# Optimization experiments

Measured on AMD Instinct MI355X. Metric: run time of the kernel, lower is better.

The kernel has to match this reference:

```python
import jax, jax.numpy as jnp
import numpy as np

# YOLOv4 stride-8 head config (yolov4.cfg)
ALL_ANCHORS = [[12,16],[19,36],[40,28],[36,75],[76,55],[72,146],[142,110],[192,243],[459,401]]
ANCHOR_MASK = [0, 1, 2]
N_CLASSES = 80
SCALE_XY = 1.2  # scale_x_y for this head
N_BBOX_ATTRS = 5  # tx, ty, tw, th, obj


def setup_inputs() -> dict:
    key = jax.random.key(0)
    attrs = N_CLASSES + N_BBOX_ATTRS  # 85
    n_anchors = len(ANCHOR_MASK)      # 3
    # raw conv output: [batch, n_anchors*attrs, grid, grid]
    x = jax.random.normal(key, (16, n_anchors * attrs, 76, 76), dtype=jnp.float32)
    return {"x": x, "input_dim": 608}


def reference(x, input_dim):
    B = x.shape[0]
    G = x.shape[2]                      # grid_dim (INPUT_H_DIM)
    stride = input_dim // G             # grid_stride
    A = len(ANCHOR_MASK)
    attrs = N_CLASSES + N_BBOX_ATTRS

    # anchors scaled to grid units: [A, 2]
    anc = jnp.asarray([ALL_ANCHORS[i] for i in ANCHOR_MASK], dtype=jnp.float32) / stride

    # [B, A, attrs, H, W] -> [B, H, W, A, attrs]
    x = x.reshape(B, A, attrs, G, G).transpose(0, 3, 4, 1, 2)

    # yolo_transform: sigmoid+scale tx/ty, exp*anchor tw/th, sigmoid obj+cls
    txy = jax.nn.sigmoid(x[..., 0:2]) * SCALE_XY - (SCALE_XY - 1.0) / 2.0
    twh = jnp.exp(x[..., 2:4]) * anc            # broadcast over [B,H,W,A,2]
    objcls = jax.nn.sigmoid(x[..., 4:])

    # add_grid_offsets: torch.meshgrid(grid, grid) is 'ij' -> y_offset[i,j]=i, x_offset[i,j]=j
    gy, gx = jnp.meshgrid(jnp.arange(G), jnp.arange(G), indexing="ij")
    off = jnp.stack([gx, gy], axis=-1).astype(jnp.float32)[:, :, None, :]  # [H,W,1,2]
    txy = txy + off

    # scale bbox attrs (tx..th) to input-image pixels
    boxes = jnp.concatenate([txy, twh], axis=-1) * jnp.float32(stride)

    out = jnp.concatenate([boxes, objcls], axis=-1)  # [B,H,W,A,attrs]
    return out.reshape(B, G * G * A, attrs)
```

## Files before the change

### kernel.cpp

```cpp
#include <hip/hip_runtime.h>

#define GRIDD  76
#define NROWS  255
#define GG     (GRIDD * GRIDD)
#define WR     16
#define WQ     (WR * 19)
#define WDW    (WR * GRIDD)

typedef __attribute__((address_space(3))) unsigned lds_u32;
typedef __attribute__((address_space(1))) unsigned glb_u32;

__device__ __forceinline__ void gll16(const float* g, float* l) {
    __builtin_amdgcn_global_load_lds((const glb_u32*)g, (lds_u32*)l, 16, 0, 0);
}

__global__ __launch_bounds__(512, 8) void yolo_head_kernel(
    const float* __restrict__ x, const int* __restrict__ dimp,
    float* __restrict__ out)
{
    __shared__ float buf[8 * WDW];
    const unsigned lb    = (blockIdx.x & 7u) * 304u + (blockIdx.x >> 3);
    const unsigned b     = lb / 152u;
    const unsigned hr    = lb - b * 152u;
    const unsigned h     = hr >> 1;
    const unsigned rbase = (hr & 1u) * 127u;
    const unsigned t     = threadIdx.x;
    const unsigned W     = t >> 6;
    const unsigned lane  = t & 63u;
    const float stride   = (float)(*dimp / GRIDD);
    const float mB       = -0.1f * stride;

    float* wbuf = buf + W * WDW;
    const unsigned wr0 = rbase + W * WR;
    const float* __restrict__ src = x + (size_t)(b * NROWS + wr0) * GG + h * GRIDD;
    #pragma unroll
    for (unsigned k = 0; k < 5u; ++k) {
        unsigned i = k * 64u + lane;
        if (i < WQ) {
            unsigned row = i / 19u;
            unsigned qc  = i - row * 19u;
            gll16(src + (size_t)row * GG + (qc << 2), wbuf + k * 256u);
        }
    }
    asm volatile("s_waitcnt vmcnt(0)" ::: "memory");

    const unsigned r    = lane & 15u;
    const unsigned rem  = wr0 + r;
    const unsigned a    = (rem >= 170u) ? 2u : ((rem >= 85u) ? 1u : 0u);
    const unsigned attr = rem - a * 85u;
    const bool  wh  = (attr == 2u) | (attr == 3u);
    const bool  isx = (attr == 0u);
    float anc = 0.f;
    if (attr == 2u) anc = (a == 0u) ? 12.f : ((a == 1u) ? 19.f : 40.f);
    if (attr == 3u) anc = (a == 0u) ? 16.f : ((a == 1u) ? 36.f : 28.f);
    const float sgn = wh ? 1.f : -1.f;
    const float A   = (attr < 2u) ? 1.2f * stride : 1.f;
    const float B0  = (attr == 1u) ? ((float)h * stride + mB) : 0.f;

    const float* lr = wbuf + r * GRIDD;
    float* __restrict__ dst = out + (size_t)(b * GRIDD + h) * (GRIDD * NROWS) + rem;

    #pragma unroll
    for (unsigned j = 0; j < 5u; ++j) {
        const unsigned qj = (lane >> 4) + (j << 2);
        if (qj < 19u) {
            const float4 vv = *reinterpret_cast<const float4*>(lr + (qj << 2));
            #pragma unroll
            for (unsigned i = 0; i < 4u; ++i) {
                const float v = (i == 0) ? vv.x : (i == 1) ? vv.y : (i == 2) ? vv.z : vv.w;
                const unsigned u = (qj << 2) + i;
                const float e   = __expf(sgn * v);
                const float sig = __builtin_amdgcn_rcpf(1.0f + e);
                const float Bi  = isx ? fmaf((float)u, stride, mB) : B0;
                const float o   = wh ? e * anc : fmaf(sig, A, Bi);
                dst[(size_t)u * NROWS] = o;
            }
        }
    }
}

extern "C" void kernel_launch(void* const* d_in, const int* in_sizes, int n_in,
                              void* d_out, int out_size, void* d_ws, size_t ws_size,
                              hipStream_t stream) {
    const float* x  = (const float*)d_in[0];
    const int* dimp = (const int*)d_in[1];
    float* out      = (float*)d_out;
    const int B = in_sizes[0] / (NROWS * GG);
    yolo_head_kernel<<<B * GRIDD * 2, 512, 0, stream>>>(x, dimp, out);
}
```

Measured before the change: 34.06 us.

## Stage block rows in two halves and overlap the second load with compute

After: 37.56 us. 10.3% more time.

```diff
diff --git a/kernel.cpp b/kernel.cpp
--- a/kernel.cpp
+++ b/kernel.cpp
@@ -3,9 +3,9 @@
 #define GRIDD  76
 #define NROWS  255
 #define GG     (GRIDD * GRIDD)
-#define WR     16
-#define WQ     (WR * 19)
-#define WDW    (WR * GRIDD)
+#define HROWS  64
+#define UPITCH 76
+#define UDW    (2 * HROWS * UPITCH)
 
 typedef __attribute__((address_space(3))) unsigned lds_u32;
 typedef __attribute__((address_space(1))) unsigned glb_u32;
@@ -14,38 +14,35 @@
     __builtin_amdgcn_global_load_lds((const glb_u32*)g, (lds_u32*)l, 16, 0, 0);
 }
 
-__global__ __launch_bounds__(512, 8) void yolo_head_kernel(
-    const float* __restrict__ x, const int* __restrict__ dimp,
-    float* __restrict__ out)
+__device__ __forceinline__ void stage_half(const float* __restrict__ src,
+                                           float* dstbase,
+                                           unsigned wid, unsigned lane)
 {
-    __shared__ float buf[8 * WDW];
-    const unsigned lb    = (blockIdx.x & 7u) * 304u + (blockIdx.x >> 3);
-    const unsigned b     = lb / 152u;
-    const unsigned hr    = lb - b * 152u;
-    const unsigned h     = hr >> 1;
-    const unsigned rbase = (hr & 1u) * 127u;
-    const unsigned t     = threadIdx.x;
-    const unsigned W     = t >> 6;
-    const unsigned lane  = t & 63u;
-    const float stride   = (float)(*dimp / GRIDD);
-    const float mB       = -0.1f * stride;
-
-    float* wbuf = buf + W * WDW;
-    const unsigned wr0 = rbase + W * WR;
-    const float* __restrict__ src = x + (size_t)(b * NROWS + wr0) * GG + h * GRIDD;
     #pragma unroll
-    for (unsigned k = 0; k < 5u; ++k) {
-        unsigned i = k * 64u + lane;
-        if (i < WQ) {
+    for (unsigned k = 0; k < 2u; ++k) {
+        unsigned i   = k * 512u + (wid << 6) + lane;
+        unsigned row = i / 19u;
+        unsigned qc  = i - row * 19u;
+        gll16(src + (size_t)row * GG + (qc << 2),
+              dstbase + (size_t)(k * 512u + (wid << 6)) * 4u);
+    }
+    {
+        unsigned i = 1024u + wid * 24u + lane;
+        if (lane < 24u) {
             unsigned row = i / 19u;
             unsigned qc  = i - row * 19u;
-            gll16(src + (size_t)row * GG + (qc << 2), wbuf + k * 256u);
+            gll16(src + (size_t)row * GG + (qc << 2),
+                  dstbase + (size_t)(1024u + wid * 24u) * 4u);
         }
     }
-    asm volatile("s_waitcnt vmcnt(0)" ::: "memory");
+}
 
-    const unsigned r    = lane & 15u;
-    const unsigned rem  = wr0 + r;
+__device__ __forceinline__ void compute_half(const float* __restrict__ bc,
+                                             float* __restrict__ outbh,
+                                             unsigned remBase, unsigned lane,
+                                             unsigned wid, float stride, float fh)
+{
+    const unsigned rem  = remBase + lane;
     const unsigned a    = (rem >= 170u) ? 2u : ((rem >= 85u) ? 1u : 0u);
     const unsigned attr = rem - a * 85u;
     const bool  wh  = (attr == 2u) | (attr == 3u);
@@ -53,30 +50,60 @@
     float anc = 0.f;
     if (attr == 2u) anc = (a == 0u) ? 12.f : ((a == 1u) ? 19.f : 40.f);
     if (attr == 3u) anc = (a == 0u) ? 16.f : ((a == 1u) ? 36.f : 28.f);
-    const float sgn = wh ? 1.f : -1.f;
-    const float A   = (attr < 2u) ? 1.2f * stride : 1.f;
-    const float B0  = (attr == 1u) ? ((float)h * stride + mB) : 0.f;
-
-    const float* lr = wbuf + r * GRIDD;
-    float* __restrict__ dst = out + (size_t)(b * GRIDD + h) * (GRIDD * NROWS) + rem;
+    const float mB    = -0.1f * stride;
+    const float slog  = wh ? 1.44269504f : -1.44269504f;
+    const float A2    = wh ? anc : ((attr < 2u) ? 1.2f * stride : 1.f);
+    const float wsel  = isx ? stride : 0.f;
+    const float basef = (attr == 1u) ? fmaf(fh, stride, mB) : (isx ? mB : 0.f);
+    float* __restrict__ dst = outbh + rem;
 
     #pragma unroll
-    for (unsigned j = 0; j < 5u; ++j) {
-        const unsigned qj = (lane >> 4) + (j << 2);
-        if (qj < 19u) {
-            const float4 vv = *reinterpret_cast<const float4*>(lr + (qj << 2));
+    for (unsigned j = 0; j < 3u; ++j) {
+        const unsigned tt = wid + (j << 3);
+        if (tt < 19u) {
+            const float4 vv = *reinterpret_cast<const float4*>(
+                bc + (size_t)lane * UPITCH + (tt << 2));
             #pragma unroll
             for (unsigned i = 0; i < 4u; ++i) {
-                const float v = (i == 0) ? vv.x : (i == 1) ? vv.y : (i == 2) ? vv.z : vv.w;
-                const unsigned u = (qj << 2) + i;
-                const float e   = __expf(sgn * v);
-                const float sig = __builtin_amdgcn_rcpf(1.0f + e);
-                const float Bi  = isx ? fmaf((float)u, stride, mB) : B0;
-                const float o   = wh ? e * anc : fmaf(sig, A, Bi);
-                dst[(size_t)u * NROWS] = o;
+                const float v  = (i == 0) ? vv.x : (i == 1) ? vv.y : (i == 2) ? vv.z : vv.w;
+                const float uf = (float)((tt << 2) + i);
+                const float e2 = exp2f(v * slog);
+                const float sg = __builtin_amdgcn_rcpf(1.0f + e2);
+                const float q  = wh ? e2 : sg;
+                const float o  = fmaf(q, A2, fmaf(uf, wsel, basef));
+                dst[(size_t)((tt << 2) + i) * NROWS] = o;
             }
         }
     }
+}
+
+__global__ __launch_bounds__(512, 8) void yolo_head_kernel(
+    const float* __restrict__ x, const int* __restrict__ dimp,
+    float* __restrict__ out)
+{
+    __shared__ float buf[UDW];
+    const unsigned lb    = (blockIdx.x & 7u) * 304u + (blockIdx.x >> 3);
+    const unsigned b     = lb / 152u;
+    const unsigned hr    = lb - b * 152u;
+    const unsigned h     = hr >> 1;
+    const unsigned rbase = (hr & 1u) * 127u;
+    const unsigned t     = threadIdx.x;
+    const unsigned wid   = t >> 6;
+    const unsigned lane  = t & 63u;
+    const float stride   = (float)(*dimp / GRIDD);
+    const float fh       = (float)h;
+
+    const float* __restrict__ src0 = x + (size_t)(b * NROWS + rbase) * GG + h * GRIDD;
+    stage_half(src0,                        buf,                  wid, lane);
+    stage_half(src0 + (size_t)HROWS * GG,   buf + HROWS * UPITCH, wid, lane);
+
+    asm volatile("s_waitcnt vmcnt(3)\n\ts_barrier" ::: "memory");
+
+    float* __restrict__ outbh = out + (size_t)(b * GRIDD + h) * (GRIDD * NROWS);
+    compute_half(buf, outbh, rbase, lane, wid, stride, fh);
+
+    __syncthreads();
+    compute_half(buf + HROWS * UPITCH, outbh, rbase + HROWS, lane, wid, stride, fh);
 }
 
 extern "C" void kernel_launch(void* const* d_in, const int* in_sizes, int n_in,
```
